# Kernel tuning notes

Hardware: AMD Instinct MI355X
Metric: run time of the kernel (lower is better)

The kernel has to match this reference:

```python
import jax, jax.numpy as jnp
import numpy as np

N_NODES = 50000
N_EDGES = 1600000
D_IN = 192   # n_features + n_graphfea
D_HID = 128


def _gcn_conv(x, W, b, src, dst, dhis, n):
    """GCNConv returning two views.
    view1: symmetric-normalized propagation with self-loops (standard GCN).
    view2: raw neighbor sum of transformed features (to be scaled by D_inv outside).
    dhis: deg_hat^{-1/2} per node, deg_hat = in-degree + 1 (self loop).
    """
    h = x @ W + b                                      # [N, hid]
    w = dhis[src] * dhis[dst]                          # [E] edge norm
    view1 = jax.ops.segment_sum(h[src] * w[:, None], dst, num_segments=n)
    view1 = view1 + h * (dhis * dhis)[:, None]         # self-loop term
    view2 = jax.ops.segment_sum(h[src], dst, num_segments=n)
    return view1, view2


def setup_inputs() -> dict:
    key = jax.random.key(0)
    ks = jax.random.split(key, 12)
    x = jax.random.normal(ks[0], (N_NODES, D_IN), dtype=jnp.float32)
    view2 = jax.random.normal(ks[1], (N_NODES, D_IN), dtype=jnp.float32)
    edge_index = jax.random.randint(ks[2], (2, N_EDGES), 0, N_NODES, dtype=jnp.int64)
    D_inv = jax.random.uniform(ks[3], (N_NODES, 1), dtype=jnp.float32)
    def glorot(k, fan_in, fan_out):
        s = jnp.sqrt(jnp.float32(2.0 / (fan_in + fan_out)))
        return jax.random.normal(k, (fan_in, fan_out), dtype=jnp.float32) * s
    W1 = glorot(ks[4], D_IN, D_HID)
    W2 = glorot(ks[5], D_HID, D_HID)
    W3 = glorot(ks[6], D_HID, D_HID)
    W4 = glorot(ks[7], D_IN, D_HID)
    W5 = glorot(ks[8], D_HID, D_HID)
    W6 = glorot(ks[9], D_HID, D_HID)
    z = jnp.zeros((D_HID,), dtype=jnp.float32)
    return {"x": x, "view2": view2, "edge_index": edge_index, "D_inv": D_inv,
            "W1": W1, "b1": z, "W2": W2, "b2": z, "W3": W3, "b3": z,
            "W4": W4, "b4": z, "W5": W5, "b5": z, "W6": W6, "b6": z}


def reference(x, view2, edge_index, D_inv,
              W1, b1, W2, b2, W3, b3, W4, b4, W5, b5, W6, b6):
    n = x.shape[0]
    src, dst = edge_index[0], edge_index[1]
    deg = jax.ops.segment_sum(jnp.ones_like(dst, dtype=x.dtype), dst, num_segments=n)
    dhis = jax.lax.rsqrt(deg + 1.0)                    # deg_hat^{-1/2}
    relu = jax.nn.relu

    x1v1, x1v2 = _gcn_conv(x, W1, b1, src, dst, dhis, n)
    x2v1, x2v2 = _gcn_conv(view2, W4, b4, src, dst, dhis, n)
    x1 = relu(x1v1 + x2v2 * D_inv)
    x2 = relu(x2v1 + x1v2 * D_inv)

    z1v1, z1v2 = _gcn_conv(x1, W2, b2, src, dst, dhis, n)
    z2v1, z2v2 = _gcn_conv(x2, W5, b5, src, dst, dhis, n)
    z1 = relu(z1v1 + z2v2 * D_inv)
    z2 = relu(z2v1 + z1v2 * D_inv)

    v1v1, v1v2 = _gcn_conv(z1, W3, b3, src, dst, dhis, n)
    v2v1, v2v2 = _gcn_conv(z2, W6, b6, src, dst, dhis, n)
    v1 = relu(v1v1 + v2v2 * D_inv)
    v2 = relu(v2v1 + v1v2 * D_inv)

    q = jnp.concatenate([x1, z1, v1], axis=1)          # [N, 3*hid]
    p = jnp.concatenate([x2, z2, v2], axis=1)
    return q, p
```

## Files before the change

kernel.cpp:

```cpp
#include <hip/hip_runtime.h>

#define N_NODES 50000
#define N_EDGES 1600000
#define D_IN 192
#define D_HID 128

#define NSLICE 8
#define SLICE_SZ ((N_NODES + NSLICE - 1) / NSLICE)

typedef __bf16 bf16x8 __attribute__((ext_vector_type(8)));
typedef float f32x4 __attribute__((ext_vector_type(4)));
typedef float f32x2 __attribute__((ext_vector_type(2)));

__device__ __forceinline__ unsigned short f2b(float x) {
    unsigned u = __builtin_bit_cast(unsigned, x);
    u += 0x7FFFu + ((u >> 16) & 1u);
    return (unsigned short)(u >> 16);
}
__device__ __forceinline__ float blo(unsigned u) {
    return __builtin_bit_cast(float, u << 16);
}
__device__ __forceinline__ float bhi(unsigned u) {
    return __builtin_bit_cast(float, u & 0xFFFF0000u);
}


__global__ void hist_kernel(const int* __restrict__ dst, int E,
                            int* __restrict__ cnt, int* __restrict__ rank) {
    int e = blockIdx.x * blockDim.x + threadIdx.x;
    if (e < E) rank[e] = atomicAdd(&cnt[dst[e]], 1);
}

__global__ __launch_bounds__(256) void scanA(const int* __restrict__ cnt,
                                             int* __restrict__ bsum, int n) {
    int i = blockIdx.x * 256 + threadIdx.x;
    int v = (i < n) ? cnt[i] : 0;
#pragma unroll
    for (int off = 32; off > 0; off >>= 1) v += __shfl_down(v, off);
    __shared__ int ws[4];
    if ((threadIdx.x & 63) == 0) ws[threadIdx.x >> 6] = v;
    __syncthreads();
    if (threadIdx.x == 0) bsum[blockIdx.x] = ws[0] + ws[1] + ws[2] + ws[3];
}

__global__ __launch_bounds__(256) void scanB(const int* __restrict__ bsum,
                                             int* __restrict__ boff,
                                             int* __restrict__ row_ptr, int nb, int n) {
    __shared__ int s[256];
    int tid = threadIdx.x;
    int v = (tid < nb) ? bsum[tid] : 0;
    s[tid] = v;
    __syncthreads();
    for (int off = 1; off < 256; off <<= 1) {
        int add = (tid >= off) ? s[tid - off] : 0;
        __syncthreads();
        s[tid] += add;
        __syncthreads();
    }
    if (tid < nb) boff[tid] = (tid > 0) ? s[tid - 1] : 0;
    if (tid == 0) row_ptr[n] = s[255];
}

__global__ __launch_bounds__(256) void scanC(const int* __restrict__ cnt,
                                             const int* __restrict__ boff,
                                             int* __restrict__ row_ptr,
                                             float* __restrict__ dhis, int n) {
    __shared__ int s[256];
    int tid = threadIdx.x;
    int i = blockIdx.x * 256 + tid;
    int c = (i < n) ? cnt[i] : 0;
    s[tid] = c;
    __syncthreads();
    for (int off = 1; off < 256; off <<= 1) {
        int add = (tid >= off) ? s[tid - off] : 0;
        __syncthreads();
        s[tid] += add;
        __syncthreads();
    }
    if (i < n) {
        int pre = boff[blockIdx.x] + s[tid] - c;
        row_ptr[i] = pre;
        dhis[i] = rsqrtf((float)c + 1.0f);
    }
}

__global__ __launch_bounds__(256) void fill_sliced(
        const int* __restrict__ src, const int* __restrict__ dst,
        const int* __restrict__ rank, const int* __restrict__ row_ptr,
        const float* __restrict__ dhis,
        int2* __restrict__ edata, int E, int nchunks) {
    int slice = blockIdx.x & (NSLICE - 1);
    int chunk = blockIdx.x >> 3;
    int lo = slice * SLICE_SZ;
    int hi = lo + SLICE_SZ;
    int per = (E + nchunks - 1) / nchunks;
    int e0 = chunk * per;
    int e1 = min(e0 + per, E);
    for (int e = e0 + threadIdx.x; e < e1; e += 256) {
        int d = dst[e];
        if (d >= lo && d < hi) {
            int s = src[e];
            edata[row_ptr[d] + rank[e]] =
                make_int2(s, __builtin_bit_cast(int, dhis[s]));
        }
    }
}


__global__ void prep_w(const float* __restrict__ W, unsigned short* __restrict__ Wt, int K) {
    int idx = blockIdx.x * 256 + threadIdx.x;
    if (idx < 128 * K) {
        int j = idx / K, k = idx - j * K;
        Wt[idx] = f2b(W[(size_t)k * 128 + j]);
    }
}


__global__ __launch_bounds__(256) void gemm_mfma(
        const float* __restrict__ A, int lda, int K, int Kp,
        const unsigned short* __restrict__ Wt, const float* __restrict__ bias,
        unsigned short* __restrict__ out, int view, int M) {
    __shared__ __align__(16) unsigned short As[64 * 200];

    int tid = threadIdx.x;
    int row0 = blockIdx.x * 64;

    {
        int r = tid >> 2;
        int q = tid & 3;
        int grow = row0 + r;
        int crow = grow < M ? grow : (M - 1);
        int kq = K >> 2;
        const float* ap = A + (size_t)crow * lda + q * kq;
        unsigned short* sp = As + r * Kp + q * kq;
        for (int k = 0; k < kq; k += 4) {
            float4 v = *(const float4*)(ap + k);
            sp[k + 0] = f2b(v.x); sp[k + 1] = f2b(v.y);
            sp[k + 2] = f2b(v.z); sp[k + 3] = f2b(v.w);
        }
    }
    __syncthreads();

    int wave = tid >> 6, lane = tid & 63;
    int m = lane & 15, quad = lane >> 4;

    f32x4 acc[8];
#pragma unroll
    for (int g = 0; g < 8; ++g) acc[g] = (f32x4){0.f, 0.f, 0.f, 0.f};

    int nsteps = K >> 5;
    for (int ks = 0; ks < nsteps; ++ks) {
        int k0 = ks * 32 + quad * 8;
        bf16x8 af = *(const bf16x8*)(As + (wave * 16 + m) * Kp + k0);
#pragma unroll
        for (int g = 0; g < 8; ++g) {
            bf16x8 bfr = *(const bf16x8*)(Wt + (size_t)(g * 16 + m) * K + k0);
            acc[g] = __builtin_amdgcn_mfma_f32_16x16x32_bf16(af, bfr, acc[g], 0, 0, 0);
        }
    }

#pragma unroll
    for (int g = 0; g < 8; ++g) {
        int col = g * 16 + m;
        float bv = bias[col];
        int ci = ((col >> 1) << 2) + (view << 1) + (col & 1);
#pragma unroll
        for (int r = 0; r < 4; ++r) {
            int grow = row0 + wave * 16 + quad * 4 + r;
            if (grow < M) out[(size_t)grow * 256 + ci] = f2b(acc[g][r] + bv);
        }
    }
}


__global__ __launch_bounds__(256) void agg_kernel(
        const unsigned* __restrict__ hcomb,
        const int* __restrict__ row_ptr, const int2* __restrict__ edata,
        const float* __restrict__ dhis, const float* __restrict__ D_inv,
        float* __restrict__ out_q, float* __restrict__ out_p, int n) {
    int wave = threadIdx.x >> 6, lane = threadIdx.x & 63;
    int d = blockIdx.x * 4 + wave;
    if (d >= n) return;

    int e0 = row_ptr[d], e1 = row_ptr[d + 1];
    f32x2 a1 = {0.f, 0.f}, g1 = {0.f, 0.f};
    f32x2 a2 = {0.f, 0.f}, g2 = {0.f, 0.f};

#define EDGE_BODY(u, w) {                                         \
        f32x2 v1 = {blo((u).x), bhi((u).x)};                      \
        f32x2 v2 = {blo((u).y), bhi((u).y)};                      \
        f32x2 wv = {(w), (w)};                                    \
        a1 += v1; g1 = __builtin_elementwise_fma(v1, wv, g1);     \
        a2 += v2; g2 = __builtin_elementwise_fma(v2, wv, g2); }

    int e = e0;
    for (; e + 4 <= e1; e += 4) {
        int4 ea = *(const int4*)(edata + e);
        int4 eb = *(const int4*)(edata + e + 2);
        uint2 u0 = *((const uint2*)(hcomb + ((size_t)ea.x << 7)) + lane);
        uint2 u1 = *((const uint2*)(hcomb + ((size_t)ea.z << 7)) + lane);
        uint2 u2 = *((const uint2*)(hcomb + ((size_t)eb.x << 7)) + lane);
        uint2 u3 = *((const uint2*)(hcomb + ((size_t)eb.z << 7)) + lane);
        float w0 = __builtin_bit_cast(float, ea.y);
        float w1 = __builtin_bit_cast(float, ea.w);
        float w2 = __builtin_bit_cast(float, eb.y);
        float w3 = __builtin_bit_cast(float, eb.w);
        EDGE_BODY(u0, w0); EDGE_BODY(u1, w1);
        EDGE_BODY(u2, w2); EDGE_BODY(u3, w3);
    }
    for (; e < e1; ++e) {
        int2 ed = edata[e];
        uint2 u = *((const uint2*)(hcomb + ((size_t)ed.x << 7)) + lane);
        float w = __builtin_bit_cast(float, ed.y);
        EDGE_BODY(u, w);
    }
#undef EDGE_BODY

    float dh = dhis[d];
    float di = D_inv[d];
    float dh2 = dh * dh;
    f32x2 dhv = {dh, dh}, dh2v = {dh2, dh2}, div = {di, di};

    uint2 us = *((const uint2*)(hcomb + ((size_t)d << 7)) + lane);
    f32x2 s1 = {blo(us.x), bhi(us.x)};
    f32x2 s2 = {blo(us.y), bhi(us.y)};

    f32x2 o1 = __builtin_elementwise_fma(g1, dhv,
               __builtin_elementwise_fma(s1, dh2v, a2 * div));
    f32x2 o2 = __builtin_elementwise_fma(g2, dhv,
               __builtin_elementwise_fma(s2, dh2v, a1 * div));

    f32x2 zero = {0.f, 0.f};
    o1 = __builtin_elementwise_max(o1, zero);
    o2 = __builtin_elementwise_max(o2, zero);
    *(f32x2*)(out_q + (size_t)d * 384 + lane * 2) = o1;
    *(f32x2*)(out_p + (size_t)d * 384 + lane * 2) = o2;
}


extern "C" void kernel_launch(void* const* d_in, const int* in_sizes, int n_in,
                              void* d_out, int out_size, void* d_ws, size_t ws_size,
                              hipStream_t stream) {
    const float* x     = (const float*)d_in[0];
    const float* view2 = (const float*)d_in[1];
    const int*   eidx  = (const int*)d_in[2];
    const float* D_inv = (const float*)d_in[3];
    const float* W1 = (const float*)d_in[4];  const float* b1 = (const float*)d_in[5];
    const float* W2 = (const float*)d_in[6];  const float* b2 = (const float*)d_in[7];
    const float* W3 = (const float*)d_in[8];  const float* b3 = (const float*)d_in[9];
    const float* W4 = (const float*)d_in[10]; const float* b4 = (const float*)d_in[11];
    const float* W5 = (const float*)d_in[12]; const float* b5 = (const float*)d_in[13];
    const float* W6 = (const float*)d_in[14]; const float* b6 = (const float*)d_in[15];

    const int n = N_NODES;
    const int E = N_EDGES;
    const int* src  = eidx;
    const int* dstv = eidx + E;

    char* ws = (char*)d_ws;
    size_t off = 0;
    auto alloc = [&](size_t bytes) -> void* {
        void* p = ws + off;
        off += (bytes + 255) & ~(size_t)255;
        return p;
    };
    int*   cnt     = (int*)alloc((size_t)n * 4);
    int*   row_ptr = (int*)alloc((size_t)(n + 1) * 4);
    float* dhis    = (float*)alloc((size_t)n * 4);
    int*   rank    = (int*)alloc((size_t)E * 4);
    int2*  edata   = (int2*)alloc((size_t)E * 8);
    int*   bsum    = (int*)alloc((size_t)256 * 4);
    int*   boff    = (int*)alloc((size_t)256 * 4);
    unsigned short* hcomb = (unsigned short*)alloc((size_t)n * 256 * 2);
    unsigned short* Wt1 = (unsigned short*)alloc((size_t)128 * 192 * 2);
    unsigned short* Wt4 = (unsigned short*)alloc((size_t)128 * 192 * 2);
    unsigned short* Wt2 = (unsigned short*)alloc((size_t)128 * 128 * 2);
    unsigned short* Wt3 = (unsigned short*)alloc((size_t)128 * 128 * 2);
    unsigned short* Wt5 = (unsigned short*)alloc((size_t)128 * 128 * 2);
    unsigned short* Wt6 = (unsigned short*)alloc((size_t)128 * 128 * 2);

    float* qb = (float*)d_out;
    float* pb = qb + (size_t)n * 384;

    hipMemsetAsync(cnt, 0, (size_t)n * 4, stream);
    int eblocks = (E + 255) / 256;
    int nb = (n + 255) / 256;
    hist_kernel<<<eblocks, 256, 0, stream>>>(dstv, E, cnt, rank);
    scanA<<<nb, 256, 0, stream>>>(cnt, bsum, n);
    scanB<<<1, 256, 0, stream>>>(bsum, boff, row_ptr, nb, n);
    scanC<<<nb, 256, 0, stream>>>(cnt, boff, row_ptr, dhis, n);
    int nchunks = 1024;
    fill_sliced<<<nchunks * NSLICE, 256, 0, stream>>>(src, dstv, rank, row_ptr,
                                                      dhis, edata, E, nchunks);

    prep_w<<<(128 * 192 + 255) / 256, 256, 0, stream>>>(W1, Wt1, 192);
    prep_w<<<(128 * 192 + 255) / 256, 256, 0, stream>>>(W4, Wt4, 192);
    prep_w<<<(128 * 128 + 255) / 256, 256, 0, stream>>>(W2, Wt2, 128);
    prep_w<<<(128 * 128 + 255) / 256, 256, 0, stream>>>(W3, Wt3, 128);
    prep_w<<<(128 * 128 + 255) / 256, 256, 0, stream>>>(W5, Wt5, 128);
    prep_w<<<(128 * 128 + 255) / 256, 256, 0, stream>>>(W6, Wt6, 128);

    int gblocks = (n + 63) / 64;
    int ablocks = (n + 3) / 4;
    const unsigned* hc = (const unsigned*)hcomb;

    gemm_mfma<<<gblocks, 256, 0, stream>>>(x,     D_IN, 192, 200, Wt1, b1, hcomb, 0, n);
    gemm_mfma<<<gblocks, 256, 0, stream>>>(view2, D_IN, 192, 200, Wt4, b4, hcomb, 1, n);
    agg_kernel<<<ablocks, 256, 0, stream>>>(hc, row_ptr, edata, dhis, D_inv, qb + 0, pb + 0, n);

    gemm_mfma<<<gblocks, 256, 0, stream>>>(qb, 384, 128, 136, Wt2, b2, hcomb, 0, n);
    gemm_mfma<<<gblocks, 256, 0, stream>>>(pb, 384, 128, 136, Wt5, b5, hcomb, 1, n);
    agg_kernel<<<ablocks, 256, 0, stream>>>(hc, row_ptr, edata, dhis, D_inv, qb + 128, pb + 128, n);

    gemm_mfma<<<gblocks, 256, 0, stream>>>(qb + 128, 384, 128, 136, Wt3, b3, hcomb, 0, n);
    gemm_mfma<<<gblocks, 256, 0, stream>>>(pb + 128, 384, 128, 136, Wt6, b6, hcomb, 1, n);
    agg_kernel<<<ablocks, 256, 0, stream>>>(hc, row_ptr, edata, dhis, D_inv, qb + 256, pb + 256, n);
}
```

Before: 881.1 us.

## Merge dual-view GEMMs, stage weights in LDS, shrink edge data to source indices

The two per-view GEMMs become one launch with a 2D grid. Weights are staged once into LDS in fragment order, and A is read directly from global memory into registers with 128 rows per block. The edge array now stores only source indices, and the aggregation loop gathers dhis per edge and unrolls by 8. The six weight-prep launches are merged into one. These changes cut launch count, edge-stream bandwidth and global weight reloads, at the cost of 48KB of LDS per block (lower occupancy) and extra random dhis gathers.

```diff
diff --git a/kernel.cpp b/kernel.cpp
--- a/kernel.cpp
+++ b/kernel.cpp
@@ -11,6 +11,7 @@
 typedef __bf16 bf16x8 __attribute__((ext_vector_type(8)));
 typedef float f32x4 __attribute__((ext_vector_type(4)));
 typedef float f32x2 __attribute__((ext_vector_type(2)));
+typedef unsigned short u16x8 __attribute__((ext_vector_type(8)));
 
 __device__ __forceinline__ unsigned short f2b(float x) {
     unsigned u = __builtin_bit_cast(unsigned, x);
@@ -22,6 +23,12 @@
 }
 __device__ __forceinline__ float bhi(unsigned u) {
     return __builtin_bit_cast(float, u & 0xFFFF0000u);
+}
+__device__ __forceinline__ bf16x8 pack8(float4 a, float4 b) {
+    u16x8 t;
+    t[0] = f2b(a.x); t[1] = f2b(a.y); t[2] = f2b(a.z); t[3] = f2b(a.w);
+    t[4] = f2b(b.x); t[5] = f2b(b.y); t[6] = f2b(b.z); t[7] = f2b(b.w);
+    return __builtin_bit_cast(bf16x8, t);
 }
 
 
@@ -87,8 +94,7 @@
 __global__ __launch_bounds__(256) void fill_sliced(
         const int* __restrict__ src, const int* __restrict__ dst,
         const int* __restrict__ rank, const int* __restrict__ row_ptr,
-        const float* __restrict__ dhis,
-        int2* __restrict__ edata, int E, int nchunks) {
+        int* __restrict__ esrc, int E, int nchunks) {
     int slice = blockIdx.x & (NSLICE - 1);
     int chunk = blockIdx.x >> 3;
     int lo = slice * SLICE_SZ;
@@ -99,75 +105,103 @@
     for (int e = e0 + threadIdx.x; e < e1; e += 256) {
         int d = dst[e];
         if (d >= lo && d < hi) {
-            int s = src[e];
-            edata[row_ptr[d] + rank[e]] =
-                make_int2(s, __builtin_bit_cast(int, dhis[s]));
+            esrc[row_ptr[d] + rank[e]] = src[e];
         }
     }
 }
 
 
-__global__ void prep_w(const float* __restrict__ W, unsigned short* __restrict__ Wt, int K) {
+__global__ void prep_all(const float* __restrict__ W1, const float* __restrict__ W4,
+                         const float* __restrict__ W2, const float* __restrict__ W3,
+                         const float* __restrict__ W5, const float* __restrict__ W6,
+                         unsigned short* __restrict__ Wt) {
     int idx = blockIdx.x * 256 + threadIdx.x;
-    if (idx < 128 * K) {
-        int j = idx / K, k = idx - j * K;
-        Wt[idx] = f2b(W[(size_t)k * 128 + j]);
-    }
-}
-
-
-__global__ __launch_bounds__(256) void gemm_mfma(
-        const float* __restrict__ A, int lda, int K, int Kp,
-        const unsigned short* __restrict__ Wt, const float* __restrict__ bias,
-        unsigned short* __restrict__ out, int view, int M) {
-    __shared__ __align__(16) unsigned short As[64 * 200];
+    const float* W; int K, base;
+    if      (idx <  24576) { W = W1; K = 192; base = 0; }
+    else if (idx <  49152) { W = W4; K = 192; base = 24576; }
+    else if (idx <  65536) { W = W2; K = 128; base = 49152; }
+    else if (idx <  81920) { W = W3; K = 128; base = 65536; }
+    else if (idx <  98304) { W = W5; K = 128; base = 81920; }
+    else if (idx < 114688) { W = W6; K = 128; base = 98304; }
+    else return;
+    int r = idx - base;
+    int j = r / K, k = r - j * K;
+    Wt[idx] = f2b(W[(size_t)k * 128 + j]);
+}
+
+
+__global__ __launch_bounds__(256) void gemm_dual(
+        const float* __restrict__ A0, const float* __restrict__ A1, int lda,
+        int K, int ns,
+        const unsigned short* __restrict__ Wt0, const unsigned short* __restrict__ Wt1,
+        const float* __restrict__ bias0, const float* __restrict__ bias1,
+        unsigned short* __restrict__ out, int M) {
+    __shared__ __align__(16) unsigned short Wlds[192 * 128];
+
+    int view = blockIdx.y;
+    const float* A = view ? A1 : A0;
+    const unsigned short* Wt = view ? Wt1 : Wt0;
+    const float* bias = view ? bias1 : bias0;
 
     int tid = threadIdx.x;
-    int row0 = blockIdx.x * 64;
-
-    {
-        int r = tid >> 2;
-        int q = tid & 3;
-        int grow = row0 + r;
-        int crow = grow < M ? grow : (M - 1);
-        int kq = K >> 2;
-        const float* ap = A + (size_t)crow * lda + q * kq;
-        unsigned short* sp = As + r * Kp + q * kq;
-        for (int k = 0; k < kq; k += 4) {
-            float4 v = *(const float4*)(ap + k);
-            sp[k + 0] = f2b(v.x); sp[k + 1] = f2b(v.y);
-            sp[k + 2] = f2b(v.z); sp[k + 3] = f2b(v.w);
-        }
+
+    int nfrag = ns * 512;
+    for (int f = tid; f < nfrag; f += 256) {
+        int lane = f & 63;
+        int gk = f >> 6;
+        int g = gk / ns, ks = gk - g * ns;
+        int col = g * 16 + (lane & 15);
+        int kpos = ks * 32 + (lane >> 4) * 8;
+        *(bf16x8*)(Wlds + (size_t)f * 8) =
+            *(const bf16x8*)(Wt + (size_t)col * K + kpos);
     }
     __syncthreads();
 
     int wave = tid >> 6, lane = tid & 63;
     int m = lane & 15, quad = lane >> 4;
-
-    f32x4 acc[8];
-#pragma unroll
-    for (int g = 0; g < 8; ++g) acc[g] = (f32x4){0.f, 0.f, 0.f, 0.f};
-
-    int nsteps = K >> 5;
-    for (int ks = 0; ks < nsteps; ++ks) {
-        int k0 = ks * 32 + quad * 8;
-        bf16x8 af = *(const bf16x8*)(As + (wave * 16 + m) * Kp + k0);
+    int row0 = blockIdx.x * 128;
+
+    int rA0 = row0 + wave * 32 + m;
+    int rA1 = rA0 + 16;
+    int cA0 = rA0 < M ? rA0 : M - 1;
+    int cA1 = rA1 < M ? rA1 : M - 1;
+    const float* a0 = A + (size_t)cA0 * lda + quad * 8;
+    const float* a1 = A + (size_t)cA1 * lda + quad * 8;
+
+    f32x4 acc[2][8];
+#pragma unroll
+    for (int h = 0; h < 2; ++h)
+#pragma unroll
+        for (int g = 0; g < 8; ++g) acc[h][g] = (f32x4){0.f, 0.f, 0.f, 0.f};
+
+    const bf16x8* wl = (const bf16x8*)Wlds;
+    for (int ks = 0; ks < ns; ++ks) {
+        float4 va = *(const float4*)(a0 + ks * 32);
+        float4 vb = *(const float4*)(a0 + ks * 32 + 4);
+        float4 vc = *(const float4*)(a1 + ks * 32);
+        float4 vd = *(const float4*)(a1 + ks * 32 + 4);
+        bf16x8 af0 = pack8(va, vb);
+        bf16x8 af1 = pack8(vc, vd);
 #pragma unroll
         for (int g = 0; g < 8; ++g) {
-            bf16x8 bfr = *(const bf16x8*)(Wt + (size_t)(g * 16 + m) * K + k0);
-            acc[g] = __builtin_amdgcn_mfma_f32_16x16x32_bf16(af, bfr, acc[g], 0, 0, 0);
+            bf16x8 bfr = wl[(g * ns + ks) * 64 + lane];
+            acc[0][g] = __builtin_amdgcn_mfma_f32_16x16x32_bf16(af0, bfr, acc[0][g], 0, 0, 0);
+            acc[1][g] = __builtin_amdgcn_mfma_f32_16x16x32_bf16(af1, bfr, acc[1][g], 0, 0, 0);
         }
     }
 
 #pragma unroll
-    for (int g = 0; g < 8; ++g) {
-        int col = g * 16 + m;
-        float bv = bias[col];
-        int ci = ((col >> 1) << 2) + (view << 1) + (col & 1);
-#pragma unroll
-        for (int r = 0; r < 4; ++r) {
-            int grow = row0 + wave * 16 + quad * 4 + r;
-            if (grow < M) out[(size_t)grow * 256 + ci] = f2b(acc[g][r] + bv);
+    for (int h = 0; h < 2; ++h) {
+#pragma unroll
+        for (int g = 0; g < 8; ++g) {
+            int col = g * 16 + m;
+            float bv = bias[col];
+            int ci = ((col >> 1) << 2) + (view << 1) + (col & 1);
+#pragma unroll
+            for (int r = 0; r < 4; ++r) {
+                int grow = row0 + wave * 32 + h * 16 + quad * 4 + r;
+                if (grow < M) out[(size_t)grow * 256 + ci] = f2b(acc[h][g][r] + bv);
+            }
         }
     }
 }
@@ -175,12 +209,14 @@
 
 __global__ __launch_bounds__(256) void agg_kernel(
         const unsigned* __restrict__ hcomb,
-        const int* __restrict__ row_ptr, const int2* __restrict__ edata,
+        const int* __restrict__ row_ptr, const int* __restrict__ esrc,
         const float* __restrict__ dhis, const float* __restrict__ D_inv,
         float* __restrict__ out_q, float* __restrict__ out_p, int n) {
     int wave = threadIdx.x >> 6, lane = threadIdx.x & 63;
     int d = blockIdx.x * 4 + wave;
     if (d >= n) return;
+
+    const uint2* hc2 = (const uint2*)hcomb;
 
     int e0 = row_ptr[d], e1 = row_ptr[d + 1];
     f32x2 a1 = {0.f, 0.f}, g1 = {0.f, 0.f};
@@ -194,25 +230,38 @@
         a2 += v2; g2 = __builtin_elementwise_fma(v2, wv, g2); }
 
     int e = e0;
-    for (; e + 4 <= e1; e += 4) {
-        int4 ea = *(const int4*)(edata + e);
-        int4 eb = *(const int4*)(edata + e + 2);
-        uint2 u0 = *((const uint2*)(hcomb + ((size_t)ea.x << 7)) + lane);
-        uint2 u1 = *((const uint2*)(hcomb + ((size_t)ea.z << 7)) + lane);
-        uint2 u2 = *((const uint2*)(hcomb + ((size_t)eb.x << 7)) + lane);
-        uint2 u3 = *((const uint2*)(hcomb + ((size_t)eb.z << 7)) + lane);
-        float w0 = __builtin_bit_cast(float, ea.y);
-        float w1 = __builtin_bit_cast(float, ea.w);
-        float w2 = __builtin_bit_cast(float, eb.y);
-        float w3 = __builtin_bit_cast(float, eb.w);
+    for (; e + 8 <= e1; e += 8) {
+        int4 sa = *(const int4*)(esrc + e);
+        int4 sb = *(const int4*)(esrc + e + 4);
+        uint2 u0 = hc2[((size_t)sa.x << 6) + lane];
+        uint2 u1 = hc2[((size_t)sa.y << 6) + lane];
+        uint2 u2 = hc2[((size_t)sa.z << 6) + lane];
+        uint2 u3 = hc2[((size_t)sa.w << 6) + lane];
+        uint2 u4 = hc2[((size_t)sb.x << 6) + lane];
+        uint2 u5 = hc2[((size_t)sb.y << 6) + lane];
+        uint2 u6 = hc2[((size_t)sb.z << 6) + lane];
+        uint2 u7 = hc2[((size_t)sb.w << 6) + lane];
+        float w0 = dhis[sa.x], w1 = dhis[sa.y], w2 = dhis[sa.z], w3 = dhis[sa.w];
+        float w4 = dhis[sb.x], w5 = dhis[sb.y], w6 = dhis[sb.z], w7 = dhis[sb.w];
         EDGE_BODY(u0, w0); EDGE_BODY(u1, w1);
         EDGE_BODY(u2, w2); EDGE_BODY(u3, w3);
+        EDGE_BODY(u4, w4); EDGE_BODY(u5, w5);
+        EDGE_BODY(u6, w6); EDGE_BODY(u7, w7);
+    }
+    for (; e + 4 <= e1; e += 4) {
+        int4 sa = *(const int4*)(esrc + e);
+        uint2 u0 = hc2[((size_t)sa.x << 6) + lane];
+        uint2 u1 = hc2[((size_t)sa.y << 6) + lane];
+        uint2 u2 = hc2[((size_t)sa.z << 6) + lane];
+        uint2 u3 = hc2[((size_t)sa.w << 6) + lane];
+        float w0 = dhis[sa.x], w1 = dhis[sa.y], w2 = dhis[sa.z], w3 = dhis[sa.w];
+        EDGE_BODY(u0, w0); EDGE_BODY(u1, w1);
+        EDGE_BODY(u2, w2); EDGE_BODY(u3, w3);
     }
     for (; e < e1; ++e) {
-        int2 ed = edata[e];
-        uint2 u = *((const uint2*)(hcomb + ((size_t)ed.x << 7)) + lane);
-        float w = __builtin_bit_cast(float, ed.y);
-        EDGE_BODY(u, w);
+        int s = esrc[e];
+        uint2 u = hc2[((size_t)s << 6) + lane];
+        EDGE_BODY(u, dhis[s]);
     }
 #undef EDGE_BODY
 
@@ -221,7 +270,7 @@
     float dh2 = dh * dh;
     f32x2 dhv = {dh, dh}, dh2v = {dh2, dh2}, div = {di, di};
 
-    uint2 us = *((const uint2*)(hcomb + ((size_t)d << 7)) + lane);
+    uint2 us = hc2[((size_t)d << 6) + lane];
     f32x2 s1 = {blo(us.x), bhi(us.x)};
     f32x2 s2 = {blo(us.y), bhi(us.y)};
 
@@ -268,16 +317,18 @@
     int*   row_ptr = (int*)alloc((size_t)(n + 1) * 4);
     float* dhis    = (float*)alloc((size_t)n * 4);
     int*   rank    = (int*)alloc((size_t)E * 4);
-    int2*  edata   = (int2*)alloc((size_t)E * 8);
+    int*   esrc    = (int*)alloc((size_t)E * 4);
     int*   bsum    = (int*)alloc((size_t)256 * 4);
     int*   boff    = (int*)alloc((size_t)256 * 4);
     unsigned short* hcomb = (unsigned short*)alloc((size_t)n * 256 * 2);
-    unsigned short* Wt1 = (unsigned short*)alloc((size_t)128 * 192 * 2);
-    unsigned short* Wt4 = (unsigned short*)alloc((size_t)128 * 192 * 2);
-    unsigned short* Wt2 = (unsigned short*)alloc((size_t)128 * 128 * 2);
-    unsigned short* Wt3 = (unsigned short*)alloc((size_t)128 * 128 * 2);
-    unsigned short* Wt5 = (unsigned short*)alloc((size_t)128 * 128 * 2);
-    unsigned short* Wt6 = (unsigned short*)alloc((size_t)128 * 128 * 2);
+    unsigned short* Wta   = (unsigned short*)alloc((size_t)114688 * 2);
+
+    unsigned short* Wt1 = Wta + 0;
+    unsigned short* Wt4 = Wta + 24576;
+    unsigned short* Wt2 = Wta + 49152;
+    unsigned short* Wt3 = Wta + 65536;
+    unsigned short* Wt5 = Wta + 81920;
+    unsigned short* Wt6 = Wta + 98304;
 
     float* qb = (float*)d_out;
     float* pb = qb + (size_t)n * 384;
@@ -291,28 +342,20 @@
     scanC<<<nb, 256, 0, stream>>>(cnt, boff, row_ptr, dhis, n);
     int nchunks = 1024;
     fill_sliced<<<nchunks * NSLICE, 256, 0, stream>>>(src, dstv, rank, row_ptr,
-                                                      dhis, edata, E, nchunks);
-
-    prep_w<<<(128 * 192 + 255) / 256, 256, 0, stream>>>(W1, Wt1, 192);
-    prep_w<<<(128 * 192 + 255) / 256, 256, 0, stream>>>(W4, Wt4, 192);
-    prep_w<<<(128 * 128 + 255) / 256, 256, 0, stream>>>(W2, Wt2, 128);
-    prep_w<<<(128 * 128 + 255) / 256, 256, 0, stream>>>(W3, Wt3, 128);
-    prep_w<<<(128 * 128 + 255) / 256, 256, 0, stream>>>(W5, Wt5, 128);
-    prep_w<<<(128 * 128 + 255) / 256, 256, 0, stream>>>(W6, Wt6, 128);
-
-    int gblocks = (n + 63) / 64;
+                                                      esrc, E, nchunks);
+
+    prep_all<<<(114688 + 255) / 256, 256, 0, stream>>>(W1, W4, W2, W3, W5, W6, Wta);
+
+    dim3 ggrid((n + 127) / 128, 2);
     int ablocks = (n + 3) / 4;
     const unsigned* hc = (const unsigned*)hcomb;
 
-    gemm_mfma<<<gblocks, 256, 0, stream>>>(x,     D_IN, 192, 200, Wt1, b1, hcomb, 0, n);
-    gemm_mfma<<<gblocks, 256, 0, stream>>>(view2, D_IN, 192, 200, Wt4, b4, hcomb, 1, n);
-    agg_kernel<<<ablocks, 256, 0, stream>>>(hc, row_ptr, edata, dhis, D_inv, qb + 0, pb + 0, n);
-
-    gemm_mfma<<<gblocks, 256, 0, stream>>>(qb, 384, 128, 136, Wt2, b2, hcomb, 0, n);
-    gemm_mfma<<<gblocks, 256, 0, stream>>>(pb, 384, 128, 136, Wt5, b5, hcomb, 1, n);
-    agg_kernel<<<ablocks, 256, 0, stream>>>(hc, row_ptr, edata, dhis, D_inv, qb + 128, pb + 128, n);
-
-    gemm_mfma<<<gblocks, 256, 0, stream>>>(qb + 128, 384, 128, 136, Wt3, b3, hcomb, 0, n);
-    gemm_mfma<<<gblocks, 256, 0, stream>>>(pb + 128, 384, 128, 136, Wt6, b6, hcomb, 1, n);
-    agg_kernel<<<ablocks, 256, 0, stream>>>(hc, row_ptr, edata, dhis, D_inv, qb + 256, pb + 256, n);
-}
+    gemm_dual<<<ggrid, 256, 0, stream>>>(x, view2, D_IN, 192, 6, Wt1, Wt4, b1, b4, hcomb, n);
+    agg_kernel<<<ablocks, 256, 0, stream>>>(hc, row_ptr, esrc, dhis, D_inv, qb + 0, pb + 0, n);
+
+    gemm_dual<<<ggrid, 256, 0, stream>>>(qb, pb, 384, 128, 4, Wt2, Wt5, b2, b5, hcomb, n);
+    agg_kernel<<<ablocks, 256, 0, stream>>>(hc, row_ptr, esrc, dhis, D_inv, qb + 128, pb + 128, n);
+
+    gemm_dual<<<ggrid, 256, 0, stream>>>(qb + 128, pb + 128, 384, 128, 4, Wt3, Wt6, b3, b6, hcomb, n);
+    agg_kernel<<<ablocks, 256, 0, stream>>>(hc, row_ptr, esrc, dhis, D_inv, qb + 256, pb + 256, n);
+}
```

Result: faster. 778.5 us (-11.6%).
